# Kernel optimization log

Hardware: AMD Instinct MI355X
Metric: run time of the kernel (lower is better)

The kernel has to match this reference:

```python
import jax, jax.numpy as jnp
import numpy as np

B, C_IN, N, T = 4, 32, 256, 256
C_OUT, K_HOPS, N_SUP, D_NV = 32, 2, 2, 10
C_MID = (K_HOPS * (N_SUP + 1) + 1) * C_OUT  # 224
NEG = jnp.float32(-1e10)


def causal_conv(x, w, b, dilation):
    # x: [B,C,N,T], w: [O,I,1,kw]; left-pad time so output length == T (causal)
    pad = (w.shape[-1] - 1) * dilation
    y = jax.lax.conv_general_dilated(
        x, w, window_strides=(1, 1), padding=[(0, 0), (pad, 0)],
        rhs_dilation=(1, dilation), dimension_numbers=('NCHW', 'OIHW', 'NCHW'))
    return y + b[None, :, None, None]


def gconv_concat(x, adjs, K):
    # K-hop diffusion over each support, concatenated on channel dim
    out = [x]
    for a in adjs:
        x1 = x
        for _ in range(K):
            x1 = jnp.einsum('ncvl,vw->ncwl', x1, a)
            out.append(x1)
    return jnp.concatenate(out, axis=1)


def mlp(h, w, b):
    # 1x1 conv: [B,Cmid,N,T] x [Cout,Cmid,1,1] -> [B,Cout,N,T]
    return jnp.einsum('ncvl,oc->novl', h, w[:, :, 0, 0]) + b[None, :, None, None]


def setup_inputs() -> dict:
    key = jax.random.key(0)
    ks = jax.random.split(key, 24)
    sc = 0.05
    r = lambda k, shape: jax.random.normal(k, shape, dtype=jnp.float32) * sc
    inp = {
        'x': jax.random.normal(ks[0], (B, C_IN, N, T), dtype=jnp.float32),
        'nodevec1': jax.random.normal(ks[1], (N, D_NV), dtype=jnp.float32),
        'nodevec2': jax.random.normal(ks[2], (D_NV, N), dtype=jnp.float32),
        'support0': jax.random.uniform(ks[3], (N, N), dtype=jnp.float32),
        'support1': jax.random.uniform(ks[4], (N, N), dtype=jnp.float32),
        'w_f1': r(ks[5], (C_OUT, C_IN, 1, 2)), 'b_f1': r(ks[6], (C_OUT,)),
        'w_g1': r(ks[7], (C_OUT, C_IN, 1, 2)), 'b_g1': r(ks[8], (C_OUT,)),
        'w_f2': r(ks[9], (C_OUT, C_OUT, 1, 2)), 'b_f2': r(ks[10], (C_OUT,)),
        'w_g2': r(ks[11], (C_OUT, C_OUT, 1, 2)), 'b_g2': r(ks[12], (C_OUT,)),
        'w_m1': r(ks[13], (C_OUT, C_MID, 1, 1)), 'b_m1': r(ks[14], (C_OUT,)),
        'w_m2': r(ks[15], (C_OUT, C_MID, 1, 1)), 'b_m2': r(ks[16], (C_OUT,)),
    }
    return inp


def reference(x, nodevec1, nodevec2, support0, support1,
              w_f1, b_f1, w_g1, b_g1, w_f2, b_f2, w_g2, b_g2,
              w_m1, b_m1, w_m2, b_m2):
    # adaptive adjacency: relu(mm) with zeros masked to -1e10, row softmax
    a = jax.nn.relu(nodevec1 @ nodevec2)
    adp = jax.nn.softmax(jnp.where(a == 0, NEG, a), axis=1)
    adjs = [support0, support1, adp]

    # block 1: dilated(1) causal gated conv + K-hop diffusion + 1x1 conv
    h = causal_conv(x, w_f1, b_f1, 1) * jax.nn.sigmoid(causal_conv(x, w_g1, b_g1, 1))
    h = mlp(gconv_concat(h, adjs, K_HOPS), w_m1, b_m1)

    # block 2: dilated(2) causal gated conv + K-hop diffusion + 1x1 conv
    h = causal_conv(h, w_f2, b_f2, 2) * jax.nn.sigmoid(causal_conv(h, w_g2, b_g2, 2))
    h = mlp(gconv_concat(h, adjs, K_HOPS), w_m2, b_m2)
    return h
```

## Files before the change

kernel.cpp:

```cpp
#include <hip/hip_runtime.h>
#include <hip/hip_bf16.h>
#include <stdint.h>

typedef unsigned short u16;
typedef __attribute__((ext_vector_type(8))) short short8;
typedef __attribute__((ext_vector_type(4))) short short4a;
typedef __attribute__((ext_vector_type(4))) float f32x4;

__device__ __forceinline__ float bf2f(u16 b){ union {unsigned u; float f;} v; v.u = ((unsigned)b)<<16; return v.f; }
__device__ __forceinline__ u16 f2bf(float f){ union {unsigned u; float f;} v; v.f = f; unsigned r = v.u + 0x7FFF + ((v.u>>16)&1); return (u16)(r>>16); }

__device__ __forceinline__ size_t bpidx(int s, int mat, int w, int v){
  return ((size_t)(((s*2+mat)*8 + (v>>5))*16 + (w>>4)))*512 + (((v>>3)&3)*16 + (w&15))*8 + (v&7);
}

__global__ __launch_bounds__(256) void k_adpw(const float* __restrict__ nv1, const float* __restrict__ nv2,
                                              float* __restrict__ adp,
                                              const float* __restrict__ wm1, const float* __restrict__ wm2,
                                              const float* __restrict__ wf1, const float* __restrict__ wg1,
                                              const float* __restrict__ wf2, const float* __restrict__ wg2,
                                              u16* __restrict__ whi, u16* __restrict__ wlo,
                                              u16* __restrict__ wcp){
  int bid = blockIdx.x;
  if(bid < 256){
    int row = bid; int j = threadIdx.x;
    float s = 0.f;
    #pragma unroll
    for(int k=0;k<10;k++) s = fmaf(nv1[row*10+k], nv2[k*256+j], s);
    s = s > 0.f ? s : 0.f;
    float val = (s == 0.f) ? -1e10f : s;
    __shared__ float red[256];
    red[j] = val; __syncthreads();
    for(int off=128; off>0; off>>=1){ if(j<off) red[j] = fmaxf(red[j], red[j+off]); __syncthreads(); }
    float mx = red[0]; __syncthreads();
    float e = __expf(val - mx);
    red[j] = e; __syncthreads();
    for(int off=128; off>0; off>>=1){ if(j<off) red[j] += red[j+off]; __syncthreads(); }
    adp[row*256+j] = e / red[0];
  } else {
    int idx = (bid-256)*256 + threadIdx.x;
    if(idx < 14336){
      float w = (idx < 7168) ? wm1[idx] : wm2[idx-7168];
      u16 hh = f2bf(w);
      whi[idx] = hh;
      wlo[idx] = f2bf(w - bf2f(hh));
    } else if(idx < 22528){
      int e = idx - 14336;
      int blk = e >> 12; int rem = e & 4095;
      int row = rem >> 6; int kk = rem & 63;
      int tap = kk >> 5; int i = kk & 31; int o = row & 31;
      const float* wsrc = blk ? (row<32 ? wf2 : wg2) : (row<32 ? wf1 : wg1);
      float w = wsrc[(o*32+i)*2 + tap];
      u16 hh = f2bf(w);
      wcp[blk*8192 + 0    + rem] = hh;
      wcp[blk*8192 + 4096 + rem] = f2bf(w - bf2f(hh));
    }
  }
}

__global__ __launch_bounds__(256) void k_badj(const float* __restrict__ s0, const float* __restrict__ s1,
                                              const float* __restrict__ adp, u16* __restrict__ badj,
                                              u16* __restrict__ bpack){
  int s = blockIdx.x >> 8; int w = blockIdx.x & 255; int v = threadIdx.x;
  const float* src = s==0 ? s0 : (s==1 ? s1 : adp);
  u16 val = f2bf(src[v*256 + w]);
  badj[(s<<16) + (w<<8) + v] = val;
  bpack[bpidx(s, 0, w, v)] = val;
}

__global__ __launch_bounds__(256) void k_tin(const float* __restrict__ x, u16* __restrict__ xT){
  int tile = blockIdx.x & 15; int slice = blockIdx.x >> 4;
  int b = slice >> 5, c = slice & 31;
  int tn0 = (tile & 3) * 64;
  int tt0 = (tile >> 2) * 64;
  const float* src = x + (size_t)slice*65536;
  __shared__ float l[64][65];
  int cc = threadIdx.x & 63, r0 = threadIdx.x >> 6;
  #pragma unroll
  for(int k=0;k<16;k++){ int r = r0 + 4*k;
    l[r][cc] = src[(size_t)(tn0 + r)*256 + tt0 + cc];
  }
  __syncthreads();
  #pragma unroll
  for(int k=0;k<16;k++){ int r = r0 + 4*k;
    xT[(((size_t)b*256 + (tt0+r))*32 + c)*256 + tn0 + cc] = f2bf(l[cc][r]);
  }
}

__global__ __launch_bounds__(256) void k_asq(const u16* __restrict__ badj,
                                             const float* __restrict__ s0, const float* __restrict__ s1,
                                             const float* __restrict__ adp, u16* __restrict__ bpack){
  __shared__ __align__(16) u16 lds[16384];
  int tid = threadIdx.x, bid = blockIdx.x;
  int s = bid >> 2, rt = bid & 3;
  int w0 = rt << 6;
  const u16* T = badj + (s<<16);
  const float* S = s==0 ? s0 : (s==1 ? s1 : adp);
  #pragma unroll
  for(int i=0;i<8;i++){
    int off = i*4096 + tid*16;
    int row = off >> 9;
    int P = (off >> 4) & 31;
    int L = (P & 16) | ((P & 15) ^ (row & 15));
    short8 v = *(const short8*)((const char*)T + (size_t)(w0 + row)*512 + L*16);
    *(short8*)((char*)lds + off) = v;
  }
  __syncthreads();
  int lane = tid & 63, wave = tid >> 6;
  int wr = (wave >> 1) << 5, wc = (wave & 1) << 7;
  f32x4 acc[2][8];
  #pragma unroll
  for(int a=0;a<2;a++)
    #pragma unroll
    for(int q=0;q<8;q++) acc[a][q] = {0.f,0.f,0.f,0.f};
  for(int ks=0; ks<8; ks++){
    short8 afr[2], bfr[8];
    #pragma unroll
    for(int mf=0; mf<2; mf++){
      int row = wr + mf*16 + (lane & 15);
      int L = ks*4 + (lane >> 4);
      int P = (L & 16) | ((L & 15) ^ (row & 15));
      afr[mf] = *(const short8*)&lds[row*256 + P*8];
    }
    #pragma unroll
    for(int nf=0; nf<8; nf++){
      int col = wc + nf*16 + (lane & 15);
      const float* src = S + (size_t)col*256 + ks*32 + (lane>>4)*8;
      #pragma unroll
      for(int jj=0;jj<8;jj++) bfr[nf][jj] = (short)f2bf(src[jj]);
    }
    #pragma unroll
    for(int mf=0;mf<2;mf++)
      #pragma unroll
      for(int nf=0;nf<8;nf++)
        acc[mf][nf] = __builtin_amdgcn_mfma_f32_16x16x32_bf16(afr[mf], bfr[nf], acc[mf][nf], 0,0,0);
  }
  #pragma unroll
  for(int mf=0;mf<2;mf++)
    #pragma unroll
    for(int nf=0;nf<8;nf++)
      #pragma unroll
      for(int rr=0;rr<4;rr++){
        int w = w0 + wr + mf*16 + (lane>>4)*4 + rr;
        int v = wc + nf*16 + (lane&15);
        bpack[bpidx(s, 1, w, v)] = f2bf(acc[mf][nf][rr]);
      }
}

template<int HILO>
__global__ __launch_bounds__(256) void k_cv(const u16* __restrict__ X0, const u16* __restrict__ X1,
                                            const u16* __restrict__ wcp, int blk, int dil,
                                            const float* __restrict__ bfv, const float* __restrict__ bgv,
                                            u16* __restrict__ outh){
  __shared__ __align__(16) u16 pl[(1+HILO)*2*8192];
  const int NPART = 1+HILO;
  int tid = threadIdx.x, bid = blockIdx.x;
  int b = bid >> 8, t = bid & 255;
  size_t base_cur = ((size_t)(b*256 + t))*8192;
  const u16* Xs[2] = {X0, X1};
  #pragma unroll
  for(int part=0; part<NPART; part++){
    #pragma unroll
    for(int tap=0; tap<2; tap++){
      bool valid = (tap==1) || (t >= dil);
      const u16* src = Xs[part] + base_cur - (tap==0 ? (size_t)dil*8192 : 0);
      char* pb = (char*)pl + (tap*NPART + part)*16384;
      #pragma unroll
      for(int it=0; it<4; it++){
        int off = it*4096 + tid*16;
        int c = off >> 9;
        int byte = off & 511;
        short8 v = {0,0,0,0,0,0,0,0};
        if(valid) v = *(const short8*)(src + (off>>1));
        *(short8*)(pb + c*512 + (byte ^ ((c&24)<<2))) = v;
      }
    }
  }
  int lane = tid & 63, wave = tid >> 6;
  const u16* wb = wcp + blk*8192;
  short8 wfr[4][2][2];
  #pragma unroll
  for(int ot=0;ot<4;ot++)
    #pragma unroll
    for(int ks=0;ks<2;ks++)
      #pragma unroll
      for(int p=0;p<2;p++)
        wfr[ot][ks][p] = *(const short8*)(wb + p*4096 + (ot*16 + (lane&15))*64 + ks*32 + (lane>>4)*8);
  __syncthreads();

  f32x4 acc[4][4];
  #pragma unroll
  for(int a=0;a<4;a++)
    #pragma unroll
    for(int q=0;q<4;q++) acc[a][q] = {0.f,0.f,0.f,0.f};
  int nbase = wave << 6;
  #pragma unroll
  for(int nf=0; nf<4; nf++){
    int n = nbase + nf*16 + (lane & 15);
    #pragma unroll
    for(int ks=0; ks<2; ks++){
      short8 xv[NPART];
      #pragma unroll
      for(int p=0;p<NPART;p++){
        char* pb = (char*)pl + (ks*NPART + p)*16384;
        short8 v;
        #pragma unroll
        for(int jj=0;jj<8;jj++){
          int c = ((lane>>4)<<3) + jj;
          v[jj] = *(const short*)(pb + c*512 + ((n*2) ^ ((c&24)<<2)));
        }
        xv[p] = v;
      }
      #pragma unroll
      for(int ot=0; ot<4; ot++){
        acc[ot][nf] = __builtin_amdgcn_mfma_f32_16x16x32_bf16(wfr[ot][ks][0], xv[0], acc[ot][nf], 0,0,0);
        acc[ot][nf] = __builtin_amdgcn_mfma_f32_16x16x32_bf16(wfr[ot][ks][1], xv[0], acc[ot][nf], 0,0,0);
        if(HILO)
          acc[ot][nf] = __builtin_amdgcn_mfma_f32_16x16x32_bf16(wfr[ot][ks][0], xv[HILO], acc[ot][nf], 0,0,0);
      }
    }
  }
  u16* ob = outh + base_cur;
  #pragma unroll
  for(int ot=0; ot<2; ot++)
    #pragma unroll
    for(int nf=0; nf<4; nf++)
      #pragma unroll
      for(int rr=0; rr<4; rr++){
        int o = ot*16 + (lane>>4)*4 + rr;
        int n = nbase + nf*16 + (lane&15);
        float fv = acc[ot][nf][rr] + bfv[o];
        float gv = acc[ot+2][nf][rr] + bgv[o];
        ob[(size_t)o*256 + n] = f2bf(fv / (1.f + __expf(-gv)));
      }
}

#define LB(KS,FC) (*(const short8*)(bp + ((((KS)*16) + cg0 + (FC))<<9) + (lane<<3)))
#define MF(A,B,C) __builtin_amdgcn_mfma_f32_16x16x32_bf16((A),(B),(C),0,0,0)
#define AF(MFI,KS) (*(const short8*)&lA[(MFI*16 + nlo)*256 + (((KS*4+khi)&16)|(((KS*4+khi)&15)^((MFI*16+nlo)&15)))*8])
template<int MODE>
__global__ __launch_bounds__(256, 5) void k_fuse(const u16* __restrict__ X,
                                                 const u16* __restrict__ bpack,
                                                 const u16* __restrict__ WH, const u16* __restrict__ WL,
                                                 const float* __restrict__ bm,
                                                 float* __restrict__ m, u16* __restrict__ mbh, u16* __restrict__ mbl){
  __shared__ __align__(16) u16 lA[8192];
  __shared__ __align__(16) char lYT[9216];
  int tid = threadIdx.x, bid = blockIdx.x;
  int ch = bid & 1;
  size_t cbase = (size_t)(bid >> 1) * 8192;
  const char* Xb = (const char*)(X + cbase);
  #pragma unroll
  for(int i=0;i<4;i++){
    int off = i*4096 + tid*16;
    int row = off >> 9;
    int P = (off >> 4) & 31;
    int L = (P & 16) | ((P & 15) ^ (row & 15));
    short8 v = *(const short8*)(Xb + (size_t)row*512 + L*16);
    *(short8*)((char*)lA + off) = v;
  }
  __syncthreads();
  int lane = tid & 63, wave = tid >> 6;
  int nlo = lane & 15, khi = lane >> 4;
  int cg0 = ch*8 + wave*2;
  char* myY = lYT + wave*2304;

  f32x4 out00={0,0,0,0}, out01=out00, out10=out00, out11=out00;

  {
    int wiA = nlo*224 + khi*8;
    short8 wh0 = *(const short8*)(WH + wiA);
    short8 wl0 = *(const short8*)(WL + wiA);
    short8 wh1 = *(const short8*)(WH + wiA + 3584);
    short8 wl1 = *(const short8*)(WL + wiA + 3584);
    #pragma unroll
    for(int nf=0;nf<2;nf++){
      int n = (ch*8 + wave*2 + nf)*16 + nlo;
      short8 f; int Lc = n >> 3; int bb = (n & 7)*2;
      #pragma unroll
      for(int j=0;j<8;j++){
        int c = khi*8 + j;
        int P = (Lc & 16) | ((Lc & 15) ^ (c & 15));
        f[j] = *(const u16*)((const char*)lA + c*512 + P*16 + bb);
      }
      if(nf==0){ out00=MF(wh0,f,out00); out00=MF(wl0,f,out00); out10=MF(wh1,f,out10); out10=MF(wl1,f,out10); }
      else     { out01=MF(wh0,f,out01); out01=MF(wl0,f,out01); out11=MF(wh1,f,out11); out11=MF(wl1,f,out11); }
    }
  }

  #pragma unroll
  for(int v=0; v<6; v++){
    const u16* bp = bpack + ((size_t)v << 16);
    f32x4 h00={0,0,0,0}, h01=h00, h10=h00, h11=h00;
    short8 p0 = LB(0,0), p1 = LB(0,1);
    short8 q0 = LB(1,0), q1 = LB(1,1);
    #pragma unroll
    for(int ks=0; ks<8; ks++){
      short8 r0, r1;
      if(ks < 6){ r0 = LB(ks+2,0); r1 = LB(ks+2,1); }
      short8 a0 = AF(0,ks), a1 = AF(1,ks);
      h00 = MF(a0, p0, h00);
      h01 = MF(a0, p1, h01);
      h10 = MF(a1, p0, h10);
      h11 = MF(a1, p1, h11);
      p0 = q0; p1 = q1;
      if(ks < 6){ q0 = r0; q1 = r1; }
    }
    #pragma unroll
    for(int mf=0;mf<2;mf++)
      #pragma unroll
      for(int nf=0;nf<2;nf++){
        f32x4 hv = mf==0 ? (nf==0?h00:h01) : (nf==0?h10:h11);
        short4a wv;
        wv[0] = (short)f2bf(hv[0]); wv[1] = (short)f2bf(hv[1]);
        wv[2] = (short)f2bf(hv[2]); wv[3] = (short)f2bf(hv[3]);
        *(short4a*)(myY + (nf*16+nlo)*72 + mf*32 + khi*8) = wv;
      }
    {
      int wiA = nlo*224 + (v+1)*32 + khi*8;
      short8 wh0 = *(const short8*)(WH + wiA);
      short8 wl0 = *(const short8*)(WL + wiA);
      short8 wh1 = *(const short8*)(WH + wiA + 3584);
      short8 wl1 = *(const short8*)(WL + wiA + 3584);
      #pragma unroll
      for(int nf=0;nf<2;nf++){
        const char* rp = myY + (nf*16+nlo)*72 + khi*16;
        short4a flo = *(const short4a*)rp;
        short4a fhi = *(const short4a*)(rp + 8);
        short8 f = {flo[0],flo[1],flo[2],flo[3],fhi[0],fhi[1],fhi[2],fhi[3]};
        if(nf==0){ out00=MF(wh0,f,out00); out00=MF(wl0,f,out00); out10=MF(wh1,f,out10); out10=MF(wl1,f,out10); }
        else     { out01=MF(wh0,f,out01); out01=MF(wl0,f,out01); out11=MF(wh1,f,out11); out11=MF(wl1,f,out11); }
      }
    }
  }

  #pragma unroll
  for(int ot=0;ot<2;ot++)
    #pragma unroll
    for(int nf=0;nf<2;nf++)
      #pragma unroll
      for(int rr=0;rr<4;rr++){
        f32x4 ov = ot==0 ? (nf==0?out00:out01) : (nf==0?out10:out11);
        int o = ot*16 + khi*4 + rr;
        int n = (ch*8 + wave*2 + nf)*16 + nlo;
        float val = ov[rr] + bm[o];
        size_t a = cbase + (size_t)o*256 + n;
        if(MODE==0){
          u16 hh = f2bf(val);
          mbh[a] = hh;
          mbl[a] = f2bf(val - bf2f(hh));
        } else {
          m[a] = val;
        }
      }
}
#undef LB
#undef MF
#undef AF

__global__ __launch_bounds__(256) void k_tip(const float* __restrict__ m, float* __restrict__ dst){
  int tile = blockIdx.x & 15; int slice = blockIdx.x >> 4;
  int b = slice >> 5, o = slice & 31;
  int tn0 = (tile & 3) * 64, tt0 = (tile >> 2) * 64;
  __shared__ float l[64][65];
  int cc = threadIdx.x & 63, r0 = threadIdx.x >> 6;
  #pragma unroll
  for(int k=0;k<16;k++){ int r = r0 + 4*k;
    l[r][cc] = m[(((size_t)b*256 + (tt0+r))*32 + o)*256 + tn0 + cc];
  }
  __syncthreads();
  #pragma unroll
  for(int k=0;k<16;k++){ int r = r0 + 4*k;
    dst[(((size_t)b*32 + o)*256 + (tn0+r))*256 + tt0 + cc] = l[cc][r];
  }
}

extern "C" void kernel_launch(void* const* d_in, const int* in_sizes, int n_in,
                              void* d_out, int out_size, void* d_ws, size_t ws_size,
                              hipStream_t stream){
  (void)in_sizes; (void)n_in; (void)out_size;
  const float* x    = (const float*)d_in[0];
  const float* nv1  = (const float*)d_in[1];
  const float* nv2  = (const float*)d_in[2];
  const float* sup0 = (const float*)d_in[3];
  const float* sup1 = (const float*)d_in[4];
  const float* wf1 = (const float*)d_in[5];  const float* bf1v = (const float*)d_in[6];
  const float* wg1 = (const float*)d_in[7];  const float* bg1v = (const float*)d_in[8];
  const float* wf2 = (const float*)d_in[9];  const float* bf2v = (const float*)d_in[10];
  const float* wg2 = (const float*)d_in[11]; const float* bg2v = (const float*)d_in[12];
  const float* wm1 = (const float*)d_in[13]; const float* bm1 = (const float*)d_in[14];
  const float* wm2 = (const float*)d_in[15]; const float* bm2 = (const float*)d_in[16];
  float* out = (float*)d_out;
  char* ws = (char*)d_ws;
  const size_t MB = (size_t)1 << 20;

  u16*  badj  = (u16*)ws;
  float* adp  = (float*)(ws + 786432);
  u16*  whi   = (u16*)(ws + 1048576);
  u16*  wlo   = (u16*)(ws + 1077248);
  u16*  wcp   = (u16*)(ws + 1105920);
  u16*  bpack = (u16*)(ws + 1179648);

  int tier = (ws_size >= 100*MB) ? 0 : 1;
  u16* h   = (u16*)(ws + 2*MB);
  u16* mbh = (u16*)(ws + 18*MB);
  u16* mbl = (u16*)(ws + 34*MB);
  u16* xT;
  float *m, *tmp = nullptr;
  if(tier==0){
    m  = (float*)(ws + 50*MB);
    xT = (u16*)(ws + 82*MB);
  } else {
    xT = mbh;
    m  = out;
    tmp = (float*)(ws + 2*MB);
  }

  k_adpw<<<344,256,0,stream>>>(nv1, nv2, adp, wm1, wm2, wf1, wg1, wf2, wg2, whi, wlo, wcp);
  k_badj<<<768,256,0,stream>>>(sup0, sup1, adp, badj, bpack);
  k_asq<<<12,256,0,stream>>>(badj, sup0, sup1, adp, bpack);
  k_tin<<<2048,256,0,stream>>>(x, xT);

  k_cv<0><<<1024,256,0,stream>>>(xT, (const u16*)0, wcp, 0, 1, bf1v, bg1v, h);
  k_fuse<0><<<2048,256,0,stream>>>(h, bpack, whi, wlo, bm1, (float*)0, mbh, mbl);
  k_cv<1><<<1024,256,0,stream>>>(mbh, mbl, wcp, 1, 2, bf2v, bg2v, h);
  k_fuse<1><<<2048,256,0,stream>>>(h, bpack, whi+7168, wlo+7168, bm2, m, (u16*)0, (u16*)0);

  if(tier==0){
    k_tip<<<2048,256,0,stream>>>(m, out);
  } else {
    k_tip<<<2048,256,0,stream>>>(m, tmp);
    (void)hipMemcpyAsync(out, tmp, (size_t)32*MB, hipMemcpyDeviceToDevice, stream);
  }
}
```

Measured before the change: 187.3 us.

## Process two time slices per block in first fused diffusion kernel

Adds k_fuse2, which loads two time-slice tiles into shared memory per block so each streamed adjacency (bpack) fragment feeds twice as many MFMAs. It halves the grid, replaces the fully unrolled support loop with a rolled loop that prefetches the next support's B fragments across iterations, and fixes occupancy at 3 waves per EU. The aim is to cut global/L2 traffic for the adjacency operand, at the cost of doubled LDS use and registers per block and lower occupancy. Only the first block's fuse kernel is switched over.

```diff
diff --git a/kernel.cpp b/kernel.cpp
--- a/kernel.cpp
+++ b/kernel.cpp
@@ -235,8 +235,156 @@
       }
 }
 
+__device__ __forceinline__ short8 gathA(const u16* TB, int n, int khi){
+  short8 f; int Lc = n >> 3; int bb = (n & 7)*2;
+  #pragma unroll
+  for(int j=0;j<8;j++){
+    int c = khi*8 + j;
+    int P = (Lc & 16) | ((Lc & 15) ^ (c & 15));
+    f[j] = (short)*(const u16*)((const char*)TB + c*512 + P*16 + bb);
+  }
+  return f;
+}
+__device__ __forceinline__ short8 gathY(const char* myY, int nl, int khi){
+  const char* rp = myY + nl*72 + khi*16;
+  short4a g0 = *(const short4a*)rp;
+  short4a g1 = *(const short4a*)(rp + 8);
+  return (short8){g0[0],g0[1],g0[2],g0[3],g1[0],g1[1],g1[2],g1[3]};
+}
+
+#define MF(A,B,C) __builtin_amdgcn_mfma_f32_16x16x32_bf16((A),(B),(C),0,0,0)
+
+#define LBP(BASE,K2,FC) (*(const short8*)((BASE) + (((K2)*16 + cg0 + (FC))<<9) + (lane<<3)))
+#define AFU(U,MFI,KS) (*(const short8*)&lA[U][((MFI)*16 + nlo)*256 + ((((KS)*4+khi)&16)|((((KS)*4+khi)&15)^(((MFI)*16+nlo)&15)))*8])
+#define STEP(KS,BA,BB) \
+  { short8 a00=AFU(0,0,KS), a01=AFU(0,1,KS), a10=AFU(1,0,KS), a11=AFU(1,1,KS); \
+    hA00=MF(a00,BA,hA00); hA01=MF(a00,BB,hA01); hA10=MF(a01,BA,hA10); hA11=MF(a01,BB,hA11); \
+    hB00=MF(a10,BA,hB00); hB01=MF(a10,BB,hB01); hB10=MF(a11,BA,hB10); hB11=MF(a11,BB,hB11); \
+    if((KS)<6){ BA = LBP(bpv,(KS)+2,0); BB = LBP(bpv,(KS)+2,1); } \
+    else if(v<5){ BA = LBP(bpn,(KS)-6,0); BB = LBP(bpn,(KS)-6,1); } }
+#define MIXU(F0,F1,O00,O01,O10,O11) \
+  { short8 f0=(F0), f1=(F1); \
+    O00=MF(wh0,f0,O00); O00=MF(wl0,f0,O00); O10=MF(wh1,f0,O10); O10=MF(wl1,f0,O10); \
+    O01=MF(wh0,f1,O01); O01=MF(wl0,f1,O01); O11=MF(wh1,f1,O11); O11=MF(wl1,f1,O11); }
+__global__ __attribute__((amdgpu_flat_work_group_size(256,256), amdgpu_waves_per_eu(3,3)))
+void k_fuse2(const u16* __restrict__ X,
+             const u16* __restrict__ bpack,
+             const u16* __restrict__ WH, const u16* __restrict__ WL,
+             const float* __restrict__ bm,
+             u16* __restrict__ mbh, u16* __restrict__ mbl){
+  __shared__ __align__(16) u16 lA[2][8192];
+  __shared__ __align__(16) char lYT[2][9216];
+  int tid = threadIdx.x, bid = blockIdx.x;
+  int ch = bid & 1;
+  int tp = (bid >> 1) & 127;
+  int b  = bid >> 8;
+  size_t cb0 = ((size_t)b*256 + tp) * 8192;
+  size_t cb1 = cb0 + (size_t)128*8192;
+  #pragma unroll
+  for(int u=0;u<2;u++){
+    const char* Xb = (const char*)(X + (u ? cb1 : cb0));
+    #pragma unroll
+    for(int i=0;i<4;i++){
+      int off = i*4096 + tid*16;
+      int row = off >> 9;
+      int P = (off >> 4) & 31;
+      int L = (P & 16) | ((P & 15) ^ (row & 15));
+      short8 v = *(const short8*)(Xb + (size_t)row*512 + L*16);
+      *(short8*)((char*)&lA[u][0] + off) = v;
+    }
+  }
+  __syncthreads();
+  int lane = tid & 63, wave = tid >> 6;
+  int nlo = lane & 15, khi = lane >> 4;
+  int cg0 = ch*8 + wave*2;
+  char* myY0 = &lYT[0][0] + wave*2304;
+  char* myY1 = &lYT[1][0] + wave*2304;
+
+  f32x4 oA00={0,0,0,0}, oA01=oA00, oA10=oA00, oA11=oA00;
+  f32x4 oB00=oA00, oB01=oA00, oB10=oA00, oB11=oA00;
+
+  const u16* bpv = bpack;
+  short8 B0A = LBP(bpv,0,0), B0B = LBP(bpv,0,1);
+  short8 B1A = LBP(bpv,1,0), B1B = LBP(bpv,1,1);
+
+  {
+    int wiA = nlo*224 + khi*8;
+    short8 wh0 = *(const short8*)(WH + wiA);
+    short8 wl0 = *(const short8*)(WL + wiA);
+    short8 wh1 = *(const short8*)(WH + wiA + 3584);
+    short8 wl1 = *(const short8*)(WL + wiA + 3584);
+    int n0 = (ch*8 + wave*2)*16 + nlo;
+    MIXU(gathA(&lA[0][0], n0, khi), gathA(&lA[0][0], n0+16, khi), oA00, oA01, oA10, oA11);
+    MIXU(gathA(&lA[1][0], n0, khi), gathA(&lA[1][0], n0+16, khi), oB00, oB01, oB10, oB11);
+  }
+
+  #pragma unroll 1
+  for(int v=0; v<6; ++v){
+    const u16* bpn = bpv + 65536;
+    f32x4 hA00={0,0,0,0}, hA01=hA00, hA10=hA00, hA11=hA00;
+    f32x4 hB00=hA00, hB01=hA00, hB10=hA00, hB11=hA00;
+    STEP(0,B0A,B0B)
+    STEP(1,B1A,B1B)
+    STEP(2,B0A,B0B)
+    STEP(3,B1A,B1B)
+    STEP(4,B0A,B0B)
+    STEP(5,B1A,B1B)
+    STEP(6,B0A,B0B)
+    STEP(7,B1A,B1B)
+    #pragma unroll
+    for(int mf=0;mf<2;mf++)
+      #pragma unroll
+      for(int nf=0;nf<2;nf++){
+        f32x4 hv = mf==0 ? (nf==0?hA00:hA01) : (nf==0?hA10:hA11);
+        short4a wv;
+        wv[0]=(short)f2bf(hv[0]); wv[1]=(short)f2bf(hv[1]);
+        wv[2]=(short)f2bf(hv[2]); wv[3]=(short)f2bf(hv[3]);
+        *(short4a*)(myY0 + (nf*16+nlo)*72 + mf*32 + khi*8) = wv;
+        f32x4 gv = mf==0 ? (nf==0?hB00:hB01) : (nf==0?hB10:hB11);
+        short4a xv;
+        xv[0]=(short)f2bf(gv[0]); xv[1]=(short)f2bf(gv[1]);
+        xv[2]=(short)f2bf(gv[2]); xv[3]=(short)f2bf(gv[3]);
+        *(short4a*)(myY1 + (nf*16+nlo)*72 + mf*32 + khi*8) = xv;
+      }
+    {
+      int wiA = nlo*224 + (v+1)*32 + khi*8;
+      short8 wh0 = *(const short8*)(WH + wiA);
+      short8 wl0 = *(const short8*)(WL + wiA);
+      short8 wh1 = *(const short8*)(WH + wiA + 3584);
+      short8 wl1 = *(const short8*)(WL + wiA + 3584);
+      MIXU(gathY(myY0, nlo, khi), gathY(myY0, 16+nlo, khi), oA00, oA01, oA10, oA11);
+      MIXU(gathY(myY1, nlo, khi), gathY(myY1, 16+nlo, khi), oB00, oB01, oB10, oB11);
+    }
+    bpv = bpn;
+  }
+
+  #pragma unroll
+  for(int u=0;u<2;u++){
+    size_t cb = u ? cb1 : cb0;
+    #pragma unroll
+    for(int ot=0;ot<2;ot++)
+      #pragma unroll
+      for(int nf=0;nf<2;nf++)
+        #pragma unroll
+        for(int rr=0;rr<4;rr++){
+          f32x4 ov = u==0 ? (ot==0 ? (nf==0?oA00:oA01) : (nf==0?oA10:oA11))
+                          : (ot==0 ? (nf==0?oB00:oB01) : (nf==0?oB10:oB11));
+          int o = ot*16 + khi*4 + rr;
+          int n = (ch*8 + wave*2 + nf)*16 + nlo;
+          float val = ov[rr] + bm[o];
+          size_t a = cb + (size_t)o*256 + n;
+          u16 hh = f2bf(val);
+          mbh[a] = hh;
+          mbl[a] = f2bf(val - bf2f(hh));
+        }
+  }
+}
+#undef LBP
+#undef AFU
+#undef STEP
+#undef MIXU
+
 #define LB(KS,FC) (*(const short8*)(bp + ((((KS)*16) + cg0 + (FC))<<9) + (lane<<3)))
-#define MF(A,B,C) __builtin_amdgcn_mfma_f32_16x16x32_bf16((A),(B),(C),0,0,0)
 #define AF(MFI,KS) (*(const short8*)&lA[(MFI*16 + nlo)*256 + (((KS*4+khi)&16)|(((KS*4+khi)&15)^((MFI*16+nlo)&15)))*8])
 template<int MODE>
 __global__ __launch_bounds__(256, 5) void k_fuse(const u16* __restrict__ X,
@@ -276,13 +424,7 @@
     #pragma unroll
     for(int nf=0;nf<2;nf++){
       int n = (ch*8 + wave*2 + nf)*16 + nlo;
-      short8 f; int Lc = n >> 3; int bb = (n & 7)*2;
-      #pragma unroll
-      for(int j=0;j<8;j++){
-        int c = khi*8 + j;
-        int P = (Lc & 16) | ((Lc & 15) ^ (c & 15));
-        f[j] = *(const u16*)((const char*)lA + c*512 + P*16 + bb);
-      }
+      short8 f = gathA((const u16*)lA, n, khi);
       if(nf==0){ out00=MF(wh0,f,out00); out00=MF(wl0,f,out00); out10=MF(wh1,f,out10); out10=MF(wl1,f,out10); }
       else     { out01=MF(wh0,f,out01); out01=MF(wl0,f,out01); out11=MF(wh1,f,out11); out11=MF(wl1,f,out11); }
     }
@@ -324,10 +466,7 @@
       short8 wl1 = *(const short8*)(WL + wiA + 3584);
       #pragma unroll
       for(int nf=0;nf<2;nf++){
-        const char* rp = myY + (nf*16+nlo)*72 + khi*16;
-        short4a flo = *(const short4a*)rp;
-        short4a fhi = *(const short4a*)(rp + 8);
-        short8 f = {flo[0],flo[1],flo[2],flo[3],fhi[0],fhi[1],fhi[2],fhi[3]};
+        short8 f = gathY(myY, nf*16+nlo, khi);
         if(nf==0){ out00=MF(wh0,f,out00); out00=MF(wl0,f,out00); out10=MF(wh1,f,out10); out10=MF(wl1,f,out10); }
         else     { out01=MF(wh0,f,out01); out01=MF(wl0,f,out01); out11=MF(wh1,f,out11); out11=MF(wl1,f,out11); }
       }
@@ -355,7 +494,6 @@
       }
 }
 #undef LB
-#undef MF
 #undef AF
 
 __global__ __launch_bounds__(256) void k_tip(const float* __restrict__ m, float* __restrict__ dst){
@@ -422,7 +560,7 @@
   k_tin<<<2048,256,0,stream>>>(x, xT);
 
   k_cv<0><<<1024,256,0,stream>>>(xT, (const u16*)0, wcp, 0, 1, bf1v, bg1v, h);
-  k_fuse<0><<<2048,256,0,stream>>>(h, bpack, whi, wlo, bm1, (float*)0, mbh, mbl);
+  k_fuse2<<<1024,256,0,stream>>>(h, bpack, whi, wlo, bm1, mbh, mbl);
   k_cv<1><<<1024,256,0,stream>>>(mbh, mbl, wcp, 1, 2, bf2v, bg2v, h);
   k_fuse<1><<<2048,256,0,stream>>>(h, bpack, whi+7168, wlo+7168, bm2, m, (u16*)0, (u16*)0);
 
```

Result: slower. 240.8 us (+28.6%).
